# Kernel optimization log

Hardware: AMD Instinct MI355X
Metric: run time of the kernel (lower is better)

Reference implementation:

```python
import jax, jax.numpy as jnp
import numpy as np

SHIFT = 1  # shift_direction fixed to +1 (module draws +/-1 at random)


def setup_inputs() -> dict:
    key = jax.random.key(0)
    k1, k2 = jax.random.split(key)
    x = jax.random.normal(k1, (128, 48, 28, 28), dtype=jnp.float32)
    w = jax.random.normal(k2, (24, 96, 7), dtype=jnp.float32)  # (Cin, Cout, K) per group, shared across groups
    return {"x": x, "w": w}


def reference(x, w):
    B, H, W = 128, 28, 28
    G, CIN, COUT, K = 2, 24, 96, 7
    # x -> (B, G, Cin, H, W); the unfold/einsum is a grouped conv1d over W (axis 'm'),
    # with H (axis 'n') untouched -> fold H into the batch dim.
    x5 = x.reshape(B, G, CIN, H, W)
    xc = x5.transpose(0, 3, 1, 2, 4).reshape(B * H, G * CIN, W)  # (B*H, 48, W)
    # kernel (Cout, Cin, K); same weights for both groups -> tile to (G*Cout, Cin, K)
    kern = jnp.tile(jnp.transpose(w, (1, 0, 2)), (G, 1, 1))  # (192, 24, 7)
    y = jax.lax.conv_general_dilated(
        xc, kern, window_strides=(1,), padding=[(3, 3)],
        dimension_numbers=('NCH', 'OIH', 'NCH'), feature_group_count=G)  # (B*H, 192, W)
    y = y.reshape(B, H, G * COUT, W).transpose(0, 2, 1, 3)  # (B, 192, H, W), channels group-major = (o, i)
    return jnp.roll(y, SHIFT, axis=2)  # roll along H (original dim 2)
```

## Files before the change

### kernel.cpp

```cpp
#include <hip/hip_runtime.h>


typedef __attribute__((ext_vector_type(8))) short short8;
typedef __attribute__((ext_vector_type(4))) float float4v;

#define B_     128
#define H_     28
#define W_     28
#define CIN_   24
#define COUT_  96
#define K_     7
#define KSTEPS 6
#define NT_    6
#define MT_    7
#define HW_    784

static __device__ __forceinline__ unsigned f2bf_u(float f) {
    union { float f; unsigned u; } v; v.f = f;
    return (v.u + 0x7fffu + ((v.u >> 16) & 1u)) >> 16;
}

__global__ __launch_bounds__(384, 2)
void conv_mfma_kernel(const float* __restrict__ x,
                      const float* __restrict__ w,
                      float* __restrict__ out) {
    const int bid  = blockIdx.x;
    const int g    = bid & 1;
    const int b    = bid >> 1;
    const int tid  = threadIdx.x;
    const int lane = tid & 63;
    const int nt   = tid >> 6;
    const int cgrp = lane & 15;
    const int kgrp = lane >> 4;

    __shared__ __align__(16) char smem[32256];
    short* wbf = (short*)smem;
    short* xs0 = (short*)smem;
    short* xs1 = (short*)(smem + 6912);

    for (int i = tid; i < 4032; i += 384) {
        const float4 v = ((const float4*)w)[i];
        const unsigned lo = f2bf_u(v.x) | (f2bf_u(v.y) << 16);
        const unsigned hi = f2bf_u(v.z) | (f2bf_u(v.w) << 16);
        ((uint2*)wbf)[i] = make_uint2(lo, hi);
    }
    __syncthreads();

    const int c_out = nt * 16 + cgrp;
    short8 br[KSTEPS];
#pragma unroll
    for (int ks = 0; ks < KSTEPS; ++ks) {
        const int q = ks * 4 + kgrp;
        if (q < 21) {
            const int k   = (q * 11) >> 5;
            const int ci0 = (q - 3 * k) * 8;
#pragma unroll
            for (int j = 0; j < 8; ++j)
                br[ks][j] = wbf[((ci0 + j) * COUT_ + c_out) * K_ + k];
        } else {
#pragma unroll
            for (int j = 0; j < 8; ++j) br[ks][j] = 0;
        }
    }
    __syncthreads();

    int koff[KSTEPS];
#pragma unroll
    for (int ks = 0; ks < KSTEPS; ++ks) {
        const int q   = ks * 4 + kgrp;
        const int k   = (q * 11) >> 5;
        const int ci0 = (q - 3 * k) * 8;
        koff[ks] = k * 24 + ci0;
    }

    float* cbase = out + ((size_t)(b * 192 + g * COUT_ + c_out)) * HW_;

    float v0r[5], v1r[5];
    auto stage_load = [&](int ht) {
#pragma unroll
        for (int it = 0; it < 5; ++it) {
            const int idx = tid + it * 384;
            if (idx < 1728) {
                const int p  = idx % 36;
                const int r  = idx / 36;
                const int cp = r % 12;
                const int hl = r / 12;
                const int ws = p - 3;
                const int rsrc = (4 * ht + hl + 27) % 28;
                float a0 = 0.0f, a1 = 0.0f;
                if (ws >= 0 && ws < W_) {
                    const size_t base =
                        ((size_t)(b * 48 + g * CIN_ + cp * 2) * H_ + rsrc) * W_ + ws;
                    a0 = x[base];
                    a1 = x[base + (size_t)HW_];
                }
                v0r[it] = a0; v1r[it] = a1;
            }
        }
    };
    auto stage_write = [&](short* xs) {
#pragma unroll
        for (int it = 0; it < 5; ++it) {
            const int idx = tid + it * 384;
            if (idx < 1728) {
                const int p  = idx % 36;
                const int r  = idx / 36;
                const int cp = r % 12;
                const int hl = r / 12;
                ((unsigned*)xs)[(hl * 36 + p) * 12 + cp] =
                    f2bf_u(v0r[it]) | (f2bf_u(v1r[it]) << 16);
            }
        }
    };
    auto compute_tile = [&](const short* xs, int ht) {
#pragma unroll
        for (int mt = 0; mt < MT_; ++mt) {
            const int mA = mt * 16 + cgrp;
            const int hA = mA / 28;
            const int tA = mA - hA * 28;
            const int abase = (hA * 36 + tA) * 24;
            float4v acc = (float4v)(0.0f);
#pragma unroll
            for (int ks = 0; ks < KSTEPS; ++ks) {
                const short8 a = *(const short8*)&xs[abase + koff[ks]];
                acc = __builtin_amdgcn_mfma_f32_16x16x32_bf16(a, br[ks], acc, 0, 0, 0);
            }
            const int m0 = mt * 16 + kgrp * 4;
            const int hl = m0 / 28;
            const int t0 = m0 - hl * 28;
            const int hd = 4 * ht + hl;
            float4 v; v.x = acc[0]; v.y = acc[1]; v.z = acc[2]; v.w = acc[3];
            *(float4*)&cbase[hd * W_ + t0] = v;
        }
    };

    stage_load(0);
    stage_write(xs0);
    __syncthreads();
#pragma unroll
    for (int ht = 0; ht < 7; ++ht) {
        const short* cur = (ht & 1) ? xs1 : xs0;
        short*       nxt = (ht & 1) ? xs0 : xs1;
        if (ht < 6) stage_load(ht + 1);
        compute_tile(cur, ht);
        if (ht < 6) stage_write(nxt);
        __syncthreads();
    }
}

extern "C" void kernel_launch(void* const* d_in, const int* in_sizes, int n_in,
                              void* d_out, int out_size, void* d_ws, size_t ws_size,
                              hipStream_t stream) {
    const float* x = (const float*)d_in[0];
    const float* w = (const float*)d_in[1];
    float* out = (float*)d_out;
    conv_mfma_kernel<<<B_ * 2, 384, 0, stream>>>(x, w, out);
}
```

Before: 28.86 us.

## Switch to 32x32x16 MFMA with weights as A operand and split H tiles across blocks

Replaces the 16x16x32 MFMA tiling with 32x32x16 MFMAs. Weights now sit in registers as the A operand and pixel columns come from LDS as B, so each wave computes 32 output channels by 128 pixels. The grid is doubled by splitting the seven H tiles across two blocks per (batch, group), and the occupancy hint is raised to 3 blocks per CU. Output stores become scalar per-channel writes coalesced along pixels rather than float4 writes. This adds redundant weight conversion per block and a tail with half-padded pixel tiles.

```diff
diff --git a/kernel.cpp b/kernel.cpp
--- a/kernel.cpp
+++ b/kernel.cpp
@@ -2,36 +2,38 @@
 
 
 typedef __attribute__((ext_vector_type(8))) short short8;
-typedef __attribute__((ext_vector_type(4))) float float4v;
+typedef __attribute__((ext_vector_type(16))) float float16v;
 
 #define B_     128
 #define H_     28
 #define W_     28
-#define CIN_   24
+#define HW_    784
 #define COUT_  96
 #define K_     7
-#define KSTEPS 6
-#define NT_    6
-#define MT_    7
-#define HW_    784
+#define KQ     11
 
 static __device__ __forceinline__ unsigned f2bf_u(float f) {
     union { float f; unsigned u; } v; v.f = f;
     return (v.u + 0x7fffu + ((v.u >> 16) & 1u)) >> 16;
 }
 
-__global__ __launch_bounds__(384, 2)
+__global__ __launch_bounds__(384, 3)
 void conv_mfma_kernel(const float* __restrict__ x,
                       const float* __restrict__ w,
                       float* __restrict__ out) {
-    const int bid  = blockIdx.x;
-    const int g    = bid & 1;
-    const int b    = bid >> 1;
+    const int bid = blockIdx.x;
+    const int s   = bid & 1;
+    const int g   = (bid >> 1) & 1;
+    const int b   = bid >> 2;
+    const int ht0 = s ? 4 : 0;
+    const int ntile = s ? 3 : 4;
     const int tid  = threadIdx.x;
     const int lane = tid & 63;
-    const int nt   = tid >> 6;
-    const int cgrp = lane & 15;
-    const int kgrp = lane >> 4;
+    const int wv   = tid >> 6;
+    const int col  = lane & 31;
+    const int half = lane >> 5;
+    const int mt   = wv >> 1;
+    const int np   = wv & 1;
 
     __shared__ __align__(16) char smem[32256];
     short* wbf = (short*)smem;
@@ -40,40 +42,43 @@
 
     for (int i = tid; i < 4032; i += 384) {
         const float4 v = ((const float4*)w)[i];
-        const unsigned lo = f2bf_u(v.x) | (f2bf_u(v.y) << 16);
-        const unsigned hi = f2bf_u(v.z) | (f2bf_u(v.w) << 16);
-        ((uint2*)wbf)[i] = make_uint2(lo, hi);
+        ((uint2*)wbf)[i] = make_uint2(f2bf_u(v.x) | (f2bf_u(v.y) << 16),
+                                      f2bf_u(v.z) | (f2bf_u(v.w) << 16));
     }
     __syncthreads();
 
-    const int c_out = nt * 16 + cgrp;
-    short8 br[KSTEPS];
+    const int ch = mt * 32 + col;
+    short8 af[KQ];
 #pragma unroll
-    for (int ks = 0; ks < KSTEPS; ++ks) {
-        const int q = ks * 4 + kgrp;
+    for (int ks = 0; ks < KQ; ++ks) {
+        const int q = 2 * ks + half;
         if (q < 21) {
-            const int k   = (q * 11) >> 5;
-            const int ci0 = (q - 3 * k) * 8;
+            const int kw  = (q * 11) >> 5;
+            const int ci0 = (q - 3 * kw) * 8;
 #pragma unroll
             for (int j = 0; j < 8; ++j)
-                br[ks][j] = wbf[((ci0 + j) * COUT_ + c_out) * K_ + k];
+                af[ks][j] = wbf[((ci0 + j) * COUT_ + ch) * K_ + kw];
         } else {
 #pragma unroll
-            for (int j = 0; j < 8; ++j) br[ks][j] = 0;
+            for (int j = 0; j < 8; ++j) af[ks][j] = 0;
         }
     }
     __syncthreads();
 
-    int koff[KSTEPS];
+    int koff[KQ];
 #pragma unroll
-    for (int ks = 0; ks < KSTEPS; ++ks) {
-        const int q   = ks * 4 + kgrp;
-        const int k   = (q * 11) >> 5;
-        const int ci0 = (q - 3 * k) * 8;
-        koff[ks] = k * 24 + ci0;
+    for (int ks = 0; ks < KQ; ++ks) {
+        const int q   = 2 * ks + half;
+        const int kw  = (q * 11) >> 5;
+        const int ci0 = (q - 3 * kw) * 8;
+        koff[ks] = kw * 24 + ci0;
     }
-
-    float* cbase = out + ((size_t)(b * 192 + g * COUT_ + c_out)) * HW_;
+    const int p0  = np * 64 + col;
+    const int p1  = p0 + 32;
+    const int hl0 = p0 / 28, t0 = p0 - hl0 * 28;
+    const int hl1 = p1 / 28, t1 = p1 - hl1 * 28;
+    const int pb0 = (hl0 * 36 + t0) * 24;
+    const int pb1 = (hl1 * 36 + t1) * 24;
 
     float v0r[5], v1r[5];
     auto stage_load = [&](int ht) {
@@ -90,7 +95,7 @@
                 float a0 = 0.0f, a1 = 0.0f;
                 if (ws >= 0 && ws < W_) {
                     const size_t base =
-                        ((size_t)(b * 48 + g * CIN_ + cp * 2) * H_ + rsrc) * W_ + ws;
+                        ((size_t)(b * 48 + g * 24 + cp * 2) * H_ + rsrc) * W_ + ws;
                     a0 = x[base];
                     a1 = x[base + (size_t)HW_];
                 }
@@ -112,38 +117,43 @@
             }
         }
     };
-    auto compute_tile = [&](const short* xs, int ht) {
-#pragma unroll
-        for (int mt = 0; mt < MT_; ++mt) {
-            const int mA = mt * 16 + cgrp;
-            const int hA = mA / 28;
-            const int tA = mA - hA * 28;
-            const int abase = (hA * 36 + tA) * 24;
-            float4v acc = (float4v)(0.0f);
-#pragma unroll
-            for (int ks = 0; ks < KSTEPS; ++ks) {
-                const short8 a = *(const short8*)&xs[abase + koff[ks]];
-                acc = __builtin_amdgcn_mfma_f32_16x16x32_bf16(a, br[ks], acc, 0, 0, 0);
-            }
-            const int m0 = mt * 16 + kgrp * 4;
-            const int hl = m0 / 28;
-            const int t0 = m0 - hl * 28;
-            const int hd = 4 * ht + hl;
-            float4 v; v.x = acc[0]; v.y = acc[1]; v.z = acc[2]; v.w = acc[3];
-            *(float4*)&cbase[hd * W_ + t0] = v;
-        }
-    };
 
-    stage_load(0);
+    float* ob = out + ((size_t)(b * 192 + g * COUT_ + mt * 32 + 4 * half)) * HW_;
+
+    stage_load(ht0);
     stage_write(xs0);
     __syncthreads();
+    for (int tix = 0; tix < ntile; ++tix) {
+        const int ht = ht0 + tix;
+        const short* cur = (tix & 1) ? xs1 : xs0;
+        short*       nxt = (tix & 1) ? xs0 : xs1;
+        if (tix < ntile - 1) stage_load(ht + 1);
+
+        float16v acc0 = (float16v)(0.0f);
+        float16v acc1 = (float16v)(0.0f);
 #pragma unroll
-    for (int ht = 0; ht < 7; ++ht) {
-        const short* cur = (ht & 1) ? xs1 : xs0;
-        short*       nxt = (ht & 1) ? xs0 : xs1;
-        if (ht < 6) stage_load(ht + 1);
-        compute_tile(cur, ht);
-        if (ht < 6) stage_write(nxt);
+        for (int ks = 0; ks < KQ; ++ks) {
+            const short8 b0 = *(const short8*)&cur[pb0 + koff[ks]];
+            const short8 b1 = *(const short8*)&cur[pb1 + koff[ks]];
+            acc0 = __builtin_amdgcn_mfma_f32_32x32x16_bf16(af[ks], b0, acc0, 0, 0, 0);
+            acc1 = __builtin_amdgcn_mfma_f32_32x32x16_bf16(af[ks], b1, acc1, 0, 0, 0);
+        }
+
+        float* obt = ob + ht * 112;
+#pragma unroll
+        for (int r = 0; r < 16; ++r) {
+            const int choff = ((r & 3) + 8 * (r >> 2)) * HW_;
+            obt[choff + p0] = acc0[r];
+        }
+        if (p1 < 112) {
+#pragma unroll
+            for (int r = 0; r < 16; ++r) {
+                const int choff = ((r & 3) + 8 * (r >> 2)) * HW_;
+                obt[choff + p1] = acc1[r];
+            }
+        }
+
+        if (tix < ntile - 1) stage_write(nxt);
         __syncthreads();
     }
 }
@@ -154,5 +164,5 @@
     const float* x = (const float*)d_in[0];
     const float* w = (const float*)d_in[1];
     float* out = (float*)d_out;
-    conv_mfma_kernel<<<B_ * 2, 384, 0, stream>>>(x, w, out);
+    conv_mfma_kernel<<<B_ * 4, 384, 0, stream>>>(x, w, out);
 }
```

Result: slower. 33.31 us (+15.4%).

## Split conv into per-row-tile blocks with precomputed bf16 weight fragments

Applied to the files above, without the earlier changes.

Weight conversion and fragment packing move into a separate small kernel that writes MFMA-ready bf16 fragments to workspace. The main kernel now launches one block per (batch, group, row tile), giving 7x more blocks with less shared memory each, instead of looping over 7 tiles with a double buffer. Packed bf16 conversion uses the hardware v_cvt_pk_bf16_f32 instruction. This raises occupancy and parallelism, at the cost of an extra kernel launch and losing the software pipelining between tiles.

```diff
diff --git a/kernel.cpp b/kernel.cpp
--- a/kernel.cpp
+++ b/kernel.cpp
@@ -15,51 +15,91 @@
 #define MT_    7
 #define HW_    784
 
-static __device__ __forceinline__ unsigned f2bf_u(float f) {
+static __device__ __forceinline__ short f2bf(float f) {
     union { float f; unsigned u; } v; v.f = f;
-    return (v.u + 0x7fffu + ((v.u >> 16) & 1u)) >> 16;
+    return (short)((v.u + 0x7fffu + ((v.u >> 16) & 1u)) >> 16);
 }
 
-__global__ __launch_bounds__(384, 2)
+static __device__ __forceinline__ unsigned cvt_pk_bf16(float a, float b) {
+    unsigned r;
+    asm("v_cvt_pk_bf16_f32 %0, %1, %2" : "=v"(r) : "v"(a), "v"(b));
+    return r;
+}
+
+__global__ __launch_bounds__(64)
+void wfrag_kernel(const float* __restrict__ w, short8* __restrict__ wf) {
+    const int idx  = blockIdx.x;
+    const int ks   = idx / 6, nt = idx - ks * 6;
+    const int lane = threadIdx.x;
+    const int c    = nt * 16 + (lane & 15);
+    const int q    = ks * 4 + (lane >> 4);
+    short8 v;
+    if (q < 21) {
+        const int k   = (q * 11) >> 5;
+        const int ci0 = (q - 3 * k) * 8;
+#pragma unroll
+        for (int j = 0; j < 8; ++j)
+            v[j] = f2bf(w[(ci0 + j) * (COUT_ * K_) + c * K_ + k]);
+    } else {
+#pragma unroll
+        for (int j = 0; j < 8; ++j) v[j] = 0;
+    }
+    wf[idx * 64 + lane] = v;
+}
+
+__global__ __launch_bounds__(384, 6)
 void conv_mfma_kernel(const float* __restrict__ x,
-                      const float* __restrict__ w,
+                      const short8* __restrict__ wfg,
                       float* __restrict__ out) {
-    const int bid  = blockIdx.x;
-    const int g    = bid & 1;
-    const int b    = bid >> 1;
+    const int bid = blockIdx.x;
+    const int ht  = bid % 7;
+    const int bg  = bid / 7;
+    const int g   = bg & 1;
+    const int b   = bg >> 1;
     const int tid  = threadIdx.x;
     const int lane = tid & 63;
     const int nt   = tid >> 6;
     const int cgrp = lane & 15;
     const int kgrp = lane >> 4;
 
-    __shared__ __align__(16) char smem[32256];
-    short* wbf = (short*)smem;
-    short* xs0 = (short*)smem;
-    short* xs1 = (short*)(smem + 6912);
+    __shared__ __align__(16) short xs[4 * 36 * 24];
 
-    for (int i = tid; i < 4032; i += 384) {
-        const float4 v = ((const float4*)w)[i];
-        const unsigned lo = f2bf_u(v.x) | (f2bf_u(v.y) << 16);
-        const unsigned hi = f2bf_u(v.z) | (f2bf_u(v.w) << 16);
-        ((uint2*)wbf)[i] = make_uint2(lo, hi);
+    float v0r[5], v1r[5];
+#pragma unroll
+    for (int it = 0; it < 5; ++it) {
+        const int idx = tid + it * 384;
+        if (idx < 1728) {
+            const int p  = idx % 36;
+            const int r  = idx / 36;
+            const int cp = r % 12;
+            const int hl = r / 12;
+            const int ws = p - 3;
+            const int rsrc = (4 * ht + hl + 27) % 28;
+            float a0 = 0.0f, a1 = 0.0f;
+            if (ws >= 0 && ws < W_) {
+                const size_t base =
+                    ((size_t)(b * 48 + g * CIN_ + cp * 2) * H_ + rsrc) * W_ + ws;
+                a0 = x[base];
+                a1 = x[base + (size_t)HW_];
+            }
+            v0r[it] = a0; v1r[it] = a1;
+        }
     }
-    __syncthreads();
 
-    const int c_out = nt * 16 + cgrp;
     short8 br[KSTEPS];
 #pragma unroll
-    for (int ks = 0; ks < KSTEPS; ++ks) {
-        const int q = ks * 4 + kgrp;
-        if (q < 21) {
-            const int k   = (q * 11) >> 5;
-            const int ci0 = (q - 3 * k) * 8;
+    for (int ks = 0; ks < KSTEPS; ++ks)
+        br[ks] = wfg[(ks * NT_ + nt) * 64 + lane];
+
 #pragma unroll
-            for (int j = 0; j < 8; ++j)
-                br[ks][j] = wbf[((ci0 + j) * COUT_ + c_out) * K_ + k];
-        } else {
-#pragma unroll
-            for (int j = 0; j < 8; ++j) br[ks][j] = 0;
+    for (int it = 0; it < 5; ++it) {
+        const int idx = tid + it * 384;
+        if (idx < 1728) {
+            const int p  = idx % 36;
+            const int r  = idx / 36;
+            const int cp = r % 12;
+            const int hl = r / 12;
+            ((unsigned*)xs)[(hl * 36 + p) * 12 + cp] = cvt_pk_bf16(v0r[it], v1r[it]);
         }
     }
     __syncthreads();
@@ -73,78 +113,27 @@
         koff[ks] = k * 24 + ci0;
     }
 
+    const int c_out = nt * 16 + cgrp;
     float* cbase = out + ((size_t)(b * 192 + g * COUT_ + c_out)) * HW_;
 
-    float v0r[5], v1r[5];
-    auto stage_load = [&](int ht) {
 #pragma unroll
-        for (int it = 0; it < 5; ++it) {
-            const int idx = tid + it * 384;
-            if (idx < 1728) {
-                const int p  = idx % 36;
-                const int r  = idx / 36;
-                const int cp = r % 12;
-                const int hl = r / 12;
-                const int ws = p - 3;
-                const int rsrc = (4 * ht + hl + 27) % 28;
-                float a0 = 0.0f, a1 = 0.0f;
-                if (ws >= 0 && ws < W_) {
-                    const size_t base =
-                        ((size_t)(b * 48 + g * CIN_ + cp * 2) * H_ + rsrc) * W_ + ws;
-                    a0 = x[base];
-                    a1 = x[base + (size_t)HW_];
-                }
-                v0r[it] = a0; v1r[it] = a1;
-            }
+    for (int mt = 0; mt < MT_; ++mt) {
+        const int mA = mt * 16 + cgrp;
+        const int hA = mA / 28;
+        const int tA = mA - hA * 28;
+        const int abase = (hA * 36 + tA) * 24;
+        float4v acc = (float4v)(0.0f);
+#pragma unroll
+        for (int ks = 0; ks < KSTEPS; ++ks) {
+            const short8 a = *(const short8*)&xs[abase + koff[ks]];
+            acc = __builtin_amdgcn_mfma_f32_16x16x32_bf16(a, br[ks], acc, 0, 0, 0);
         }
-    };
-    auto stage_write = [&](short* xs) {
-#pragma unroll
-        for (int it = 0; it < 5; ++it) {
-            const int idx = tid + it * 384;
-            if (idx < 1728) {
-                const int p  = idx % 36;
-                const int r  = idx / 36;
-                const int cp = r % 12;
-                const int hl = r / 12;
-                ((unsigned*)xs)[(hl * 36 + p) * 12 + cp] =
-                    f2bf_u(v0r[it]) | (f2bf_u(v1r[it]) << 16);
-            }
-        }
-    };
-    auto compute_tile = [&](const short* xs, int ht) {
-#pragma unroll
-        for (int mt = 0; mt < MT_; ++mt) {
-            const int mA = mt * 16 + cgrp;
-            const int hA = mA / 28;
-            const int tA = mA - hA * 28;
-            const int abase = (hA * 36 + tA) * 24;
-            float4v acc = (float4v)(0.0f);
-#pragma unroll
-            for (int ks = 0; ks < KSTEPS; ++ks) {
-                const short8 a = *(const short8*)&xs[abase + koff[ks]];
-                acc = __builtin_amdgcn_mfma_f32_16x16x32_bf16(a, br[ks], acc, 0, 0, 0);
-            }
-            const int m0 = mt * 16 + kgrp * 4;
-            const int hl = m0 / 28;
-            const int t0 = m0 - hl * 28;
-            const int hd = 4 * ht + hl;
-            float4 v; v.x = acc[0]; v.y = acc[1]; v.z = acc[2]; v.w = acc[3];
-            *(float4*)&cbase[hd * W_ + t0] = v;
-        }
-    };
-
-    stage_load(0);
-    stage_write(xs0);
-    __syncthreads();
-#pragma unroll
-    for (int ht = 0; ht < 7; ++ht) {
-        const short* cur = (ht & 1) ? xs1 : xs0;
-        short*       nxt = (ht & 1) ? xs0 : xs1;
-        if (ht < 6) stage_load(ht + 1);
-        compute_tile(cur, ht);
-        if (ht < 6) stage_write(nxt);
-        __syncthreads();
+        const int m0 = mt * 16 + kgrp * 4;
+        const int hl = m0 / 28;
+        const int t0 = m0 - hl * 28;
+        const int hd = 4 * ht + hl;
+        float4 v; v.x = acc[0]; v.y = acc[1]; v.z = acc[2]; v.w = acc[3];
+        *(float4*)&cbase[hd * W_ + t0] = v;
     }
 }
 
@@ -154,5 +143,8 @@
     const float* x = (const float*)d_in[0];
     const float* w = (const float*)d_in[1];
     float* out = (float*)d_out;
-    conv_mfma_kernel<<<B_ * 2, 384, 0, stream>>>(x, w, out);
+    short8* wf = (short8*)d_ws;
+
+    wfrag_kernel<<<36, 64, 0, stream>>>(w, wf);
+    conv_mfma_kernel<<<B_ * 2 * 7, 384, 0, stream>>>(x, wf, out);
 }
```

Result: faster. 28.24 us (-2.1%).
